# Performance work log

Measured on AMD Instinct MI355X. Metric: run time of the kernel, lower is better.

Reference implementation:

```python
import jax, jax.numpy as jnp
import numpy as np

N, E = 50000, 1600000
IN_DIM, HID, L, H = 300, 256, 3, 4
HD = HID // H  # 64
EPS = 1e-5


def setup_inputs() -> dict:
    key = jax.random.key(0)
    ks = jax.random.split(key, 24)
    s = 0.02
    inp = {
        'node_feats': jax.random.normal(ks[0], (N, IN_DIM), jnp.float32),
        'role': jax.random.randint(ks[1], (N,), 0, 3),
        'edge_src': jax.random.randint(ks[2], (E,), 0, N),
        'edge_dst': jax.random.randint(ks[3], (E,), 0, N),
        'edge_weights': jax.random.uniform(ks[4], (E,), jnp.float32),
        # input role transforms (question / entity / context)
        'Wq': jax.random.normal(ks[5], (IN_DIM, HID), jnp.float32) * s,
        'bq': jnp.zeros((HID,), jnp.float32),
        'We': jax.random.normal(ks[6], (IN_DIM, HID), jnp.float32) * s,
        'be': jnp.zeros((HID,), jnp.float32),
        'Wc': jax.random.normal(ks[7], (IN_DIM, HID), jnp.float32) * s,
        'bc': jnp.zeros((HID,), jnp.float32),
        # per-head value projections [H, HID, HD] (q/k projections omitted:
        # softmax over a scalar == 1.0, so they never affect output or grads)
        'Wv': jax.random.normal(ks[8], (H, HID, HD), jnp.float32) * s,
        'bv': jnp.zeros((H, HD), jnp.float32),
        # shared 'default' edge-type transform (the torch code always falls
        # through to 'default' because edata['rel'] entries are tensors)
        'Wd': jax.random.normal(ks[9], (HD, HD), jnp.float32) * s,
        'bd': jnp.zeros((HD,), jnp.float32),
        # attention_output
        'Wo': jax.random.normal(ks[10], (HID, HID), jnp.float32) * s,
        'bo': jnp.zeros((HID,), jnp.float32),
        # GRUCell params (torch layout: [3*HID, in], gate order r,z,n)
        'W_ih': jax.random.normal(ks[11], (3 * HID, HID), jnp.float32) * s,
        'W_hh': jax.random.normal(ks[12], (3 * HID, HID), jnp.float32) * s,
        'b_ih': jnp.zeros((3 * HID,), jnp.float32),
        'b_hh': jnp.zeros((3 * HID,), jnp.float32),
        # per-layer LayerNorm affine params [L, HID]
        'ln_w': jnp.ones((L, HID), jnp.float32),
        'ln_b': jnp.zeros((L, HID), jnp.float32),
    }
    return inp


def _layernorm(x, w, b):
    mu = jnp.mean(x, -1, keepdims=True)
    var = jnp.mean(jnp.square(x - mu), -1, keepdims=True)
    return (x - mu) * jax.lax.rsqrt(var + EPS) * w + b


def _gru_cell(x, hprev, W_ih, W_hh, b_ih, b_hh):
    gi = x @ W_ih.T + b_ih
    gh = hprev @ W_hh.T + b_hh
    i_r, i_z, i_n = jnp.split(gi, 3, axis=-1)
    h_r, h_z, h_n = jnp.split(gh, 3, axis=-1)
    r = jax.nn.sigmoid(i_r + h_r)
    z = jax.nn.sigmoid(i_z + h_z)
    n = jnp.tanh(i_n + r * h_n)
    return (1.0 - z) * n + z * hprev


def reference(node_feats, role, edge_src, edge_dst, edge_weights,
              Wq, bq, We, be, Wc, bc, Wv, bv, Wd, bd, Wo, bo,
              W_ih, W_hh, b_ih, b_hh, ln_w, ln_b):
    n_nodes = node_feats.shape[0]
    # role-dependent input transform: 0=question, 1=evidence/answer, 2=other
    hq = node_feats @ Wq + bq
    he = node_feats @ We + be
    hc = node_feats @ Wc + bc
    r = role[:, None]
    h = jax.nn.relu(jnp.where(r == 0, hq, jnp.where(r == 1, he, hc)))

    path_mem = jax.lax.stop_gradient(h)  # .detach().clone()
    prev_h = h
    num_layers, num_heads = ln_w.shape[0], Wv.shape[0]
    for layer in range(num_layers):
        head_msgs = []
        for hd in range(num_heads):
            # value proj + shared 'default' edge transform (node-level, fused)
            vt = (h @ Wv[hd] + bv[hd]) @ Wd + bd  # [N, HD]
            # scalar softmax == 1.0 -> attn_weight == edge_weight
            msg = vt[edge_src] * edge_weights[:, None]  # [E, HD]
            head_msgs.append(jax.ops.segment_sum(msg, edge_dst,
                                                 num_segments=n_nodes))
        combined = jnp.concatenate(head_msgs, axis=-1)  # [N, HID]
        path_mem = _gru_cell(combined, path_mem, W_ih, W_hh, b_ih, b_hh)
        h = _layernorm(prev_h + combined @ Wo + bo, ln_w[layer], ln_b[layer])
        # dropout: identity in eval mode
        prev_h = h
    return h + path_mem
```

## Files before the change

### kernel.cpp

```cpp
#include <hip/hip_runtime.h>
#include <math.h>

#define NN 50000
#define EE 1600000
#define IND 300
#define KPAD 320
#define NL 3
#define NBLK 785
#define AGG_NB 12500

typedef unsigned short u16;
typedef __attribute__((ext_vector_type(8))) short short8;
typedef __attribute__((ext_vector_type(4))) float floatx4;

__device__ __forceinline__ float b2f(u16 u) {
  union { unsigned i; float f; } v; v.i = ((unsigned)u) << 16; return v.f;
}
__device__ __forceinline__ u16 f2b(float f) {
  union { unsigned i; float f; } v; v.f = f;
  unsigned b = v.i; b += 0x7fffu + ((b >> 16) & 1u);
  return (u16)(b >> 16);
}
__device__ __forceinline__ float sigf(float x) { return 1.0f / (1.0f + __expf(-x)); }

__global__ void count_kernel(const int* __restrict__ dst, int* __restrict__ cnt) {
  int e = blockIdx.x * 256 + threadIdx.x;
  if (e < EE) atomicAdd(&cnt[dst[e]], 1);
}

__global__ __launch_bounds__(256) void scan1_kernel(const int* __restrict__ cnt,
                                                    int* __restrict__ rs,
                                                    int* __restrict__ bsum) {
  __shared__ int ws[4];
  const int t = threadIdx.x, l = t & 63, w = t >> 6;
  const int base = blockIdx.x * 2048 + t * 8;
  int v[8];
  int tot = 0;
  #pragma unroll
  for (int k = 0; k < 8; ++k) {
    int i = base + k;
    v[k] = (i < NN) ? cnt[i] : 0;
    tot += v[k];
  }
  int x = tot;
  #pragma unroll
  for (int off = 1; off < 64; off <<= 1) {
    int y = __shfl_up(x, off);
    if (l >= off) x += y;
  }
  if (l == 63) ws[w] = x;
  __syncthreads();
  int wpre = 0;
  for (int q = 0; q < w; ++q) wpre += ws[q];
  int run = wpre + (x - tot);
  #pragma unroll
  for (int k = 0; k < 8; ++k) {
    int i = base + k;
    if (i < NN) rs[i] = run;
    run += v[k];
  }
  if (t == 255) bsum[blockIdx.x] = wpre + x;
}

__global__ void scan2_kernel(int* __restrict__ bsum, int nb) {
  int l = threadIdx.x;
  int v = (l < nb) ? bsum[l] : 0;
  int x = v;
  #pragma unroll
  for (int off = 1; off < 64; off <<= 1) {
    int y = __shfl_up(x, off);
    if (l >= off) x += y;
  }
  if (l < nb) bsum[l] = x - v;
  if (l == 63) bsum[nb] = x;
}

__global__ void scan3_kernel(const int* __restrict__ bsum, int* __restrict__ rs, int nb) {
  int i = blockIdx.x * 256 + threadIdx.x;
  if (i < NN) rs[i] += bsum[i >> 11];
  if (i == 0) rs[NN] = bsum[nb];
}

__global__ void fill_kernel(const int* __restrict__ dst, const int* __restrict__ rs,
                            int* __restrict__ ncnt, const int* __restrict__ esrc,
                            const float* __restrict__ ew, int2* __restrict__ srcw) {
  int e = blockIdx.x * 256 + threadIdx.x;
  if (e < EE) {
    int d = dst[e];
    int p = atomicAdd(&ncnt[d], 1);
    int2 v;
    v.x = esrc[e];
    v.y = __float_as_int(ew[e]);
    srcw[rs[d] + p] = v;
  }
}

__global__ void role_count(const int* __restrict__ role, int* __restrict__ cnt3) {
  __shared__ int lc[3];
  if (threadIdx.x < 3) lc[threadIdx.x] = 0;
  __syncthreads();
  int i = blockIdx.x * 256 + threadIdx.x;
  if (i < NN) atomicAdd(&lc[role[i]], 1);
  __syncthreads();
  if (threadIdx.x < 3) atomicAdd(&cnt3[threadIdx.x], lc[threadIdx.x]);
}

__global__ void role_plan(const int* __restrict__ cnt3, int* __restrict__ pbase,
                          int* __restrict__ blkrole) {
  __shared__ int pb[4];
  if (threadIdx.x == 0) {
    pb[0] = 0;
    for (int b = 0; b < 3; ++b) pb[b + 1] = pb[b] + (((cnt3[b] + 63) >> 6) << 6);
    for (int b = 0; b < 4; ++b) pbase[b] = pb[b];
  }
  __syncthreads();
  for (int blk = threadIdx.x; blk < NBLK; blk += 256) {
    int m0 = blk * 64;
    int r = -1;
    for (int b = 0; b < 3; ++b)
      if (m0 >= pb[b] && m0 < pb[b + 1]) r = b;
    blkrole[blk] = r;
  }
}

__global__ void role_fill(const int* __restrict__ role, const int* __restrict__ pbase,
                          int* __restrict__ pos3, int* __restrict__ perm) {
  __shared__ int lcnt[3], lbase[3];
  int i = blockIdx.x * 256 + threadIdx.x;
  if (threadIdx.x < 3) lcnt[threadIdx.x] = 0;
  __syncthreads();
  int r = 0, lr = 0;
  bool valid = (i < NN);
  if (valid) {
    r = role[i];
    lr = atomicAdd(&lcnt[r], 1);
  }
  __syncthreads();
  if (threadIdx.x < 3) lbase[threadIdx.x] = atomicAdd(&pos3[threadIdx.x], lcnt[threadIdx.x]);
  __syncthreads();
  if (valid) perm[pbase[r] + lbase[r] + lr] = i;
}

__global__ void xcast_kernel(const float* __restrict__ X, u16* __restrict__ Xb) {
  size_t i = (size_t)blockIdx.x * 256 + threadIdx.x;
  if (i >= (size_t)NN * KPAD) return;
  int r = (int)(i / KPAD), k = (int)(i % KPAD);
  Xb[i] = (k < IND) ? f2b(X[(size_t)r * IND + k]) : (u16)0;
}

__global__ void wt3_kernel(const float* __restrict__ Wq, const float* __restrict__ We,
                           const float* __restrict__ Wc, u16* __restrict__ Wqt,
                           u16* __restrict__ Wet, u16* __restrict__ Wct) {
  int n = blockIdx.x;
  int which = blockIdx.y;
  const float* W = (which == 0) ? Wq : (which == 1) ? We : Wc;
  u16* Wt = (which == 0) ? Wqt : (which == 1) ? Wet : Wct;
  for (int k = threadIdx.x; k < KPAD; k += 256)
    Wt[(size_t)n * KPAD + k] = (k < IND) ? f2b(W[(size_t)k * 256 + n]) : (u16)0;
}

__global__ void wallt_kernel(const float* __restrict__ Wv, const float* __restrict__ Wd,
                             u16* __restrict__ Wallt) {
  int i = blockIdx.x;
  int c = threadIdx.x;
  int hd = c >> 6, j = c & 63;
  const float* wv = &Wv[hd * (256 * 64) + i * 64];
  float s = 0.f;
  #pragma unroll
  for (int m = 0; m < 64; ++m) s = fmaf(wv[m], Wd[m * 64 + j], s);
  Wallt[(size_t)c * 256 + i] = f2b(s);
}

__global__ void ball_kernel(const float* __restrict__ bv, const float* __restrict__ Wd,
                            const float* __restrict__ bd, float* __restrict__ ball) {
  int c = threadIdx.x;
  int hd = c >> 6, j = c & 63;
  float s = bd[j];
  #pragma unroll
  for (int m = 0; m < 64; ++m) s = fmaf(bv[hd * 64 + m], Wd[m * 64 + j], s);
  ball[c] = s;
}

__global__ void wot_kernel(const float* __restrict__ Wo, u16* __restrict__ Wot) {
  int n = blockIdx.x;
  int k = threadIdx.x;
  Wot[(size_t)n * 256 + k] = f2b(Wo[(size_t)k * 256 + n]);
}

__global__ void castbf2_kernel(const float* __restrict__ s0, const float* __restrict__ s1,
                               u16* __restrict__ d0, u16* __restrict__ d1) {
  int i = blockIdx.x * 256 + threadIdx.x;
  const int n = 768 * 256;
  if (i < n) d0[i] = f2b(s0[i]);
  else if (i < 2 * n) d1[i - n] = f2b(s1[i - n]);
}

#define GEMM_PROLOG \
  __shared__ __align__(16) u16 As[64][72]; \
  __shared__ __align__(16) u16 Bs[64][72]; \
  const int t = threadIdx.x; \
  const int lane = t & 63; \
  const int wv_ = t >> 6; \
  const int wr = wv_ >> 1, wc = wv_ & 1; \
  const int l15 = lane & 15, l4 = lane >> 4; \
  const int srow = t >> 2; \
  const int scol = (t & 3) << 4;

#define STAGE_A(AG, ASTRIDE, VALID, ROWIDX, K0) { \
  int4 v0 = {0, 0, 0, 0}, v1 = {0, 0, 0, 0}; \
  if (VALID) { \
    const int4* p_ = (const int4*)&(AG)[(size_t)(ROWIDX) * (ASTRIDE) + (K0) + scol]; \
    v0 = p_[0]; v1 = p_[1]; \
  } \
  *(int4*)&As[srow][scol] = v0; \
  *(int4*)&As[srow][scol + 8] = v1; }

#define STAGE_B(BG, BSTRIDE, ROWIDX, K0) { \
  const int4* p_ = (const int4*)&(BG)[(size_t)(ROWIDX) * (BSTRIDE) + (K0) + scol]; \
  *(int4*)&Bs[srow][scol] = p_[0]; \
  *(int4*)&Bs[srow][scol + 8] = p_[1]; }

#define MFMA_STEP(ACC) { \
  _Pragma("unroll") \
  for (int kc = 0; kc < 2; ++kc) { \
    short8 a0_ = *(const short8*)&As[wr * 32 + 0 + l15][kc * 32 + l4 * 8]; \
    short8 a1_ = *(const short8*)&As[wr * 32 + 16 + l15][kc * 32 + l4 * 8]; \
    short8 b0_ = *(const short8*)&Bs[wc * 32 + 0 + l15][kc * 32 + l4 * 8]; \
    short8 b1_ = *(const short8*)&Bs[wc * 32 + 16 + l15][kc * 32 + l4 * 8]; \
    ACC[0][0] = __builtin_amdgcn_mfma_f32_16x16x32_bf16(a0_, b0_, ACC[0][0], 0, 0, 0); \
    ACC[0][1] = __builtin_amdgcn_mfma_f32_16x16x32_bf16(a0_, b1_, ACC[0][1], 0, 0, 0); \
    ACC[1][0] = __builtin_amdgcn_mfma_f32_16x16x32_bf16(a1_, b0_, ACC[1][0], 0, 0, 0); \
    ACC[1][1] = __builtin_amdgcn_mfma_f32_16x16x32_bf16(a1_, b1_, ACC[1][1], 0, 0, 0); \
  } }

#define GEMM128_PROLOG \
  __shared__ __align__(16) u16 As[128][72]; \
  __shared__ __align__(16) u16 Bs[128][72]; \
  const int t = threadIdx.x; \
  const int lane = t & 63; \
  const int wv_ = t >> 6; \
  const int qr = (wv_ >> 1) * 64, qc = (wv_ & 1) * 64; \
  const int l15 = lane & 15, l4 = lane >> 4; \
  const int srow = t >> 1; \
  const int scol = (t & 1) * 32;

#define STAGE128_A(AG, ASTRIDE, VALID, ROWIDX, K0) { \
  int4 v0 = {0,0,0,0}, v1 = {0,0,0,0}, v2 = {0,0,0,0}, v3 = {0,0,0,0}; \
  if (VALID) { \
    const int4* p_ = (const int4*)&(AG)[(size_t)(ROWIDX) * (ASTRIDE) + (K0) + scol]; \
    v0 = p_[0]; v1 = p_[1]; v2 = p_[2]; v3 = p_[3]; \
  } \
  *(int4*)&As[srow][scol] = v0; *(int4*)&As[srow][scol + 8] = v1; \
  *(int4*)&As[srow][scol + 16] = v2; *(int4*)&As[srow][scol + 24] = v3; }

#define STAGE128_B(BG, BSTRIDE, ROWIDX, K0) { \
  const int4* p_ = (const int4*)&(BG)[(size_t)(ROWIDX) * (BSTRIDE) + (K0) + scol]; \
  *(int4*)&Bs[srow][scol] = p_[0]; *(int4*)&Bs[srow][scol + 8] = p_[1]; \
  *(int4*)&Bs[srow][scol + 16] = p_[2]; *(int4*)&Bs[srow][scol + 24] = p_[3]; }

#define MFMA128_STEP(ACC) { \
  _Pragma("unroll") \
  for (int kc = 0; kc < 2; ++kc) { \
    short8 af_[4], bf_[4]; \
    _Pragma("unroll") \
    for (int m = 0; m < 4; ++m) af_[m] = *(const short8*)&As[qr + m * 16 + l15][kc * 32 + l4 * 8]; \
    _Pragma("unroll") \
    for (int n = 0; n < 4; ++n) bf_[n] = *(const short8*)&Bs[qc + n * 16 + l15][kc * 32 + l4 * 8]; \
    _Pragma("unroll") \
    for (int m = 0; m < 4; ++m) \
      _Pragma("unroll") \
      for (int n = 0; n < 4; ++n) \
        ACC[m][n] = __builtin_amdgcn_mfma_f32_16x16x32_bf16(af_[m], bf_[n], ACC[m][n], 0, 0, 0); \
  } }

__global__ __launch_bounds__(256) void proj_mfma(
    const u16* __restrict__ Xb, const int* __restrict__ perm,
    const int* __restrict__ blkrole,
    const u16* __restrict__ Wqt, const u16* __restrict__ Wet, const u16* __restrict__ Wct,
    const float* __restrict__ bq, const float* __restrict__ be, const float* __restrict__ bc,
    u16* __restrict__ h, u16* __restrict__ pm) {
  const int brole = blkrole[blockIdx.y];
  if (brole < 0) return;
  GEMM_PROLOG
  const int m0 = blockIdx.y * 64;
  const int n0 = blockIdx.x * 64;
  const u16* Bt = (brole == 0) ? Wqt : (brole == 1) ? Wet : Wct;
  const float* bb = (brole == 0) ? bq : (brole == 1) ? be : bc;
  const int prow = perm[m0 + srow];
  floatx4 acc[2][2] = {};
  for (int k0 = 0; k0 < KPAD; k0 += 64) {
    STAGE_A(Xb, KPAD, prow >= 0, prow, k0)
    STAGE_B(Bt, KPAD, n0 + srow, k0)
    __syncthreads();
    MFMA_STEP(acc)
    __syncthreads();
  }
  #pragma unroll
  for (int m = 0; m < 2; ++m)
    #pragma unroll
    for (int reg = 0; reg < 4; ++reg) {
      int gr = m0 + wr * 32 + m * 16 + l4 * 4 + reg;
      int pr = perm[gr];
      if (pr >= 0) {
        #pragma unroll
        for (int n = 0; n < 2; ++n) {
          int c = n0 + wc * 32 + n * 16 + l15;
          float vo = fmaxf(acc[m][n][reg] + bb[c], 0.f);
          u16 ub = f2b(vo);
          h[(size_t)pr * 256 + c] = ub;
          pm[(size_t)pr * 256 + c] = ub;
        }
      }
    }
}

__global__ __launch_bounds__(256) void vgemm_mfma(
    const u16* __restrict__ A, const u16* __restrict__ Bt,
    const float* __restrict__ bias, u16* __restrict__ Vs) {
  GEMM128_PROLOG
  const int m0 = blockIdx.y * 128;
  const int n0 = blockIdx.x * 128;
  const int ar = m0 + srow;
  floatx4 acc[4][4] = {};
  for (int k0 = 0; k0 < 256; k0 += 64) {
    STAGE128_A(A, 256, ar < NN, ar, k0)
    STAGE128_B(Bt, 256, n0 + srow, k0)
    __syncthreads();
    MFMA128_STEP(acc)
    __syncthreads();
  }
  #pragma unroll
  for (int m = 0; m < 4; ++m)
    #pragma unroll
    for (int reg = 0; reg < 4; ++reg) {
      int gr = m0 + qr + m * 16 + l4 * 4 + reg;
      if (gr < NN) {
        #pragma unroll
        for (int n = 0; n < 4; ++n) {
          int c = n0 + qc + n * 16 + l15;
          size_t off = ((size_t)(c >> 5) * NN + gr) * 32 + (c & 31);
          Vs[off] = f2b(acc[m][n][reg] + bias[c]);
        }
      }
    }
}

__global__ __launch_bounds__(256) void agg_kernel(
    const int2* __restrict__ srcw, const int* __restrict__ rs,
    const u16* __restrict__ Vs, u16* __restrict__ comb) {
  int bid = blockIdx.x;
  int slice = bid / AGG_NB;
  int nb = bid - slice * AGG_NB;
  int n = nb * 4 + (threadIdx.x >> 6);
  int lane = threadIdx.x & 63;
  int hh = lane >> 5;
  int u = lane & 31;
  int s = rs[n], e = rs[n + 1];
  const u16* __restrict__ vbase = Vs + (size_t)slice * NN * 32;
  float a0 = 0.f, a1 = 0.f, a2 = 0.f, a3 = 0.f;
  for (int base = s; base < e; base += 64) {
    int2 p = {0, 0};
    if (base + lane < e) p = srcw[base + lane];
    int cnt = min(64, e - base);
    for (int k = 0; k < cnt; k += 8) {
      int j0 = k + hh, j1 = k + 2 + hh, j2 = k + 4 + hh, j3 = k + 6 + hh;
      int s0 = __shfl(p.x, j0 & 63), s1 = __shfl(p.x, j1 & 63);
      int s2 = __shfl(p.x, j2 & 63), s3 = __shfl(p.x, j3 & 63);
      int w0i = __shfl(p.y, j0 & 63), w1i = __shfl(p.y, j1 & 63);
      int w2i = __shfl(p.y, j2 & 63), w3i = __shfl(p.y, j3 & 63);
      bool v0 = j0 < cnt, v1 = j1 < cnt, v2 = j2 < cnt, v3 = j3 < cnt;
      float w0 = v0 ? __int_as_float(w0i) : 0.f;
      float w1 = v1 ? __int_as_float(w1i) : 0.f;
      float w2 = v2 ? __int_as_float(w2i) : 0.f;
      float w3 = v3 ? __int_as_float(w3i) : 0.f;
      s0 = v0 ? s0 : 0; s1 = v1 ? s1 : 0;
      s2 = v2 ? s2 : 0; s3 = v3 ? s3 : 0;
      float f0 = b2f(vbase[(size_t)s0 * 32 + u]);
      float f1 = b2f(vbase[(size_t)s1 * 32 + u]);
      float f2 = b2f(vbase[(size_t)s2 * 32 + u]);
      float f3 = b2f(vbase[(size_t)s3 * 32 + u]);
      a0 = fmaf(w0, f0, a0); a1 = fmaf(w1, f1, a1);
      a2 = fmaf(w2, f2, a2); a3 = fmaf(w3, f3, a3);
    }
  }
  float a = (a0 + a1) + (a2 + a3);
  a += __shfl_xor(a, 32);
  if (hh == 0) comb[(size_t)n * 256 + slice * 32 + u] = f2b(a);
}

__global__ __launch_bounds__(256) void gru_mfma(
    const u16* __restrict__ comb, const u16* __restrict__ pmc,
    const u16* __restrict__ Wiht, const u16* __restrict__ Whht,
    const float* __restrict__ bih, const float* __restrict__ bhh,
    u16* __restrict__ pmn) {
  __shared__ __align__(16) u16 As[2][64][72];
  __shared__ __align__(16) u16 Bs[6][64][72];
  const int t = threadIdx.x;
  const int lane = t & 63;
  const int wv_ = t >> 6;
  const int wr = wv_ >> 1, wc = wv_ & 1;
  const int l15 = lane & 15, l4 = lane >> 4;
  const int srow = t >> 2;
  const int scol = (t & 3) << 4;
  const int m0 = blockIdx.y * 64;
  const int cb = blockIdx.x;
  const int ar = m0 + srow;
  const bool av = ar < NN;
  floatx4 acc[6][2][2] = {};
  for (int k0 = 0; k0 < 256; k0 += 64) {
    {
      int4 v0 = {0,0,0,0}, v1 = {0,0,0,0}, u0 = {0,0,0,0}, u1 = {0,0,0,0};
      if (av) {
        const int4* pa = (const int4*)&comb[(size_t)ar * 256 + k0 + scol];
        v0 = pa[0]; v1 = pa[1];
        const int4* pb = (const int4*)&pmc[(size_t)ar * 256 + k0 + scol];
        u0 = pb[0]; u1 = pb[1];
      }
      *(int4*)&As[0][srow][scol] = v0; *(int4*)&As[0][srow][scol + 8] = v1;
      *(int4*)&As[1][srow][scol] = u0; *(int4*)&As[1][srow][scol + 8] = u1;
    }
    #pragma unroll
    for (int g = 0; g < 3; ++g) {
      size_t row = (size_t)(g * 256 + cb * 64 + srow);
      const int4* p1 = (const int4*)&Wiht[row * 256 + k0 + scol];
      *(int4*)&Bs[g][srow][scol] = p1[0];
      *(int4*)&Bs[g][srow][scol + 8] = p1[1];
      const int4* p2 = (const int4*)&Whht[row * 256 + k0 + scol];
      *(int4*)&Bs[3 + g][srow][scol] = p2[0];
      *(int4*)&Bs[3 + g][srow][scol + 8] = p2[1];
    }
    __syncthreads();
    #pragma unroll
    for (int kc = 0; kc < 2; ++kc) {
      short8 a0f[2], a1f[2];
      #pragma unroll
      for (int m = 0; m < 2; ++m) {
        a0f[m] = *(const short8*)&As[0][wr * 32 + m * 16 + l15][kc * 32 + l4 * 8];
        a1f[m] = *(const short8*)&As[1][wr * 32 + m * 16 + l15][kc * 32 + l4 * 8];
      }
      #pragma unroll
      for (int g = 0; g < 3; ++g) {
        short8 b0 = *(const short8*)&Bs[g][wc * 32 + 0 + l15][kc * 32 + l4 * 8];
        short8 b1 = *(const short8*)&Bs[g][wc * 32 + 16 + l15][kc * 32 + l4 * 8];
        acc[g][0][0] = __builtin_amdgcn_mfma_f32_16x16x32_bf16(a0f[0], b0, acc[g][0][0], 0, 0, 0);
        acc[g][0][1] = __builtin_amdgcn_mfma_f32_16x16x32_bf16(a0f[0], b1, acc[g][0][1], 0, 0, 0);
        acc[g][1][0] = __builtin_amdgcn_mfma_f32_16x16x32_bf16(a0f[1], b0, acc[g][1][0], 0, 0, 0);
        acc[g][1][1] = __builtin_amdgcn_mfma_f32_16x16x32_bf16(a0f[1], b1, acc[g][1][1], 0, 0, 0);
      }
      #pragma unroll
      for (int g = 3; g < 6; ++g) {
        short8 b0 = *(const short8*)&Bs[g][wc * 32 + 0 + l15][kc * 32 + l4 * 8];
        short8 b1 = *(const short8*)&Bs[g][wc * 32 + 16 + l15][kc * 32 + l4 * 8];
        acc[g][0][0] = __builtin_amdgcn_mfma_f32_16x16x32_bf16(a1f[0], b0, acc[g][0][0], 0, 0, 0);
        acc[g][0][1] = __builtin_amdgcn_mfma_f32_16x16x32_bf16(a1f[0], b1, acc[g][0][1], 0, 0, 0);
        acc[g][1][0] = __builtin_amdgcn_mfma_f32_16x16x32_bf16(a1f[1], b0, acc[g][1][0], 0, 0, 0);
        acc[g][1][1] = __builtin_amdgcn_mfma_f32_16x16x32_bf16(a1f[1], b1, acc[g][1][1], 0, 0, 0);
      }
    }
    __syncthreads();
  }
  #pragma unroll
  for (int m = 0; m < 2; ++m)
    #pragma unroll
    for (int reg = 0; reg < 4; ++reg) {
      int gr = m0 + wr * 32 + m * 16 + l4 * 4 + reg;
      if (gr < NN) {
        #pragma unroll
        for (int n = 0; n < 2; ++n) {
          int c = cb * 64 + wc * 32 + n * 16 + l15;
          float r = sigf(acc[0][m][n][reg] + acc[3][m][n][reg] + bih[c] + bhh[c]);
          float z = sigf(acc[1][m][n][reg] + acc[4][m][n][reg] + bih[256 + c] + bhh[256 + c]);
          float i_n = acc[2][m][n][reg] + bih[512 + c];
          float h_n = acc[5][m][n][reg] + bhh[512 + c];
          float nn2 = tanhf(i_n + r * h_n);
          float po = b2f(pmc[(size_t)gr * 256 + c]);
          pmn[(size_t)gr * 256 + c] = f2b((1.f - z) * nn2 + z * po);
        }
      }
    }
}

__global__ __launch_bounds__(256) void wo_mfma(
    const u16* __restrict__ comb, const u16* __restrict__ Wot,
    const float* __restrict__ bo, const u16* __restrict__ h,
    u16* __restrict__ tmp) {
  GEMM128_PROLOG
  const int m0 = blockIdx.y * 128;
  const int n0 = blockIdx.x * 128;
  const int ar = m0 + srow;
  floatx4 acc[4][4] = {};
  for (int k0 = 0; k0 < 256; k0 += 64) {
    STAGE128_A(comb, 256, ar < NN, ar, k0)
    STAGE128_B(Wot, 256, n0 + srow, k0)
    __syncthreads();
    MFMA128_STEP(acc)
    __syncthreads();
  }
  #pragma unroll
  for (int m = 0; m < 4; ++m)
    #pragma unroll
    for (int reg = 0; reg < 4; ++reg) {
      int gr = m0 + qr + m * 16 + l4 * 4 + reg;
      if (gr < NN) {
        #pragma unroll
        for (int n = 0; n < 4; ++n) {
          int c = n0 + qc + n * 16 + l15;
          float v = acc[m][n][reg] + bo[c] + b2f(h[(size_t)gr * 256 + c]);
          tmp[(size_t)gr * 256 + c] = f2b(v);
        }
      }
    }
}

__global__ __launch_bounds__(256) void ln_kernel(
    const u16* __restrict__ tmp, u16* __restrict__ h,
    const float* __restrict__ lnw, const float* __restrict__ lnb) {
  int n = blockIdx.x * 4 + (threadIdx.x >> 6);
  int l = threadIdx.x & 63;
  if (n >= NN) return;
  ushort4 v = *(const ushort4*)&tmp[(size_t)n * 256 + l * 4];
  float x0 = b2f(v.x), x1 = b2f(v.y), x2 = b2f(v.z), x3 = b2f(v.w);
  float s = x0 + x1 + x2 + x3;
  #pragma unroll
  for (int off = 1; off < 64; off <<= 1) s += __shfl_xor(s, off);
  float mu = s * (1.f / 256.f);
  float d0 = x0 - mu, d1 = x1 - mu, d2 = x2 - mu, d3 = x3 - mu;
  float vs = d0 * d0 + d1 * d1 + d2 * d2 + d3 * d3;
  #pragma unroll
  for (int off = 1; off < 64; off <<= 1) vs += __shfl_xor(vs, off);
  float inv = rsqrtf(vs * (1.f / 256.f) + 1e-5f);
  int c = l * 4;
  ushort4 o;
  o.x = f2b(d0 * inv * lnw[c + 0] + lnb[c + 0]);
  o.y = f2b(d1 * inv * lnw[c + 1] + lnb[c + 1]);
  o.z = f2b(d2 * inv * lnw[c + 2] + lnb[c + 2]);
  o.w = f2b(d3 * inv * lnw[c + 3] + lnb[c + 3]);
  *(ushort4*)&h[(size_t)n * 256 + c] = o;
}

__global__ __launch_bounds__(256) void ln_final_kernel(
    const u16* __restrict__ tmp, const u16* __restrict__ pm,
    const float* __restrict__ lnw, const float* __restrict__ lnb,
    float* __restrict__ out) {
  int n = blockIdx.x * 4 + (threadIdx.x >> 6);
  int l = threadIdx.x & 63;
  if (n >= NN) return;
  ushort4 v = *(const ushort4*)&tmp[(size_t)n * 256 + l * 4];
  float x0 = b2f(v.x), x1 = b2f(v.y), x2 = b2f(v.z), x3 = b2f(v.w);
  float s = x0 + x1 + x2 + x3;
  #pragma unroll
  for (int off = 1; off < 64; off <<= 1) s += __shfl_xor(s, off);
  float mu = s * (1.f / 256.f);
  float d0 = x0 - mu, d1 = x1 - mu, d2 = x2 - mu, d3 = x3 - mu;
  float vs = d0 * d0 + d1 * d1 + d2 * d2 + d3 * d3;
  #pragma unroll
  for (int off = 1; off < 64; off <<= 1) vs += __shfl_xor(vs, off);
  float inv = rsqrtf(vs * (1.f / 256.f) + 1e-5f);
  int c = l * 4;
  ushort4 pv = *(const ushort4*)&pm[(size_t)n * 256 + c];
  float4 o;
  o.x = b2f(f2b(d0 * inv * lnw[c + 0] + lnb[c + 0])) + b2f(pv.x);
  o.y = b2f(f2b(d1 * inv * lnw[c + 1] + lnb[c + 1])) + b2f(pv.y);
  o.z = b2f(f2b(d2 * inv * lnw[c + 2] + lnb[c + 2])) + b2f(pv.z);
  o.w = b2f(f2b(d3 * inv * lnw[c + 3] + lnb[c + 3])) + b2f(pv.w);
  *(float4*)&out[(size_t)n * 256 + c] = o;
}

extern "C" void kernel_launch(void* const* d_in, const int* in_sizes, int n_in,
                              void* d_out, int out_size, void* d_ws, size_t ws_size,
                              hipStream_t stream) {
  const float* node_feats = (const float*)d_in[0];
  const int* role = (const int*)d_in[1];
  const int* esrc = (const int*)d_in[2];
  const int* edst = (const int*)d_in[3];
  const float* ew = (const float*)d_in[4];
  const float* Wq = (const float*)d_in[5];
  const float* bq = (const float*)d_in[6];
  const float* We = (const float*)d_in[7];
  const float* be = (const float*)d_in[8];
  const float* Wc = (const float*)d_in[9];
  const float* bc = (const float*)d_in[10];
  const float* Wv = (const float*)d_in[11];
  const float* bv = (const float*)d_in[12];
  const float* Wd = (const float*)d_in[13];
  const float* bd = (const float*)d_in[14];
  const float* Wo = (const float*)d_in[15];
  const float* bo = (const float*)d_in[16];
  const float* Wih = (const float*)d_in[17];
  const float* Whh = (const float*)d_in[18];
  const float* bih = (const float*)d_in[19];
  const float* bhh = (const float*)d_in[20];
  const float* lnw = (const float*)d_in[21];
  const float* lnb = (const float*)d_in[22];
  float* out = (float*)d_out;

  char* ws = (char*)d_ws;
  size_t off = 0;
  auto take = [&](size_t bytes) {
    char* p = ws + off;
    off = (off + bytes + 511) & ~(size_t)511;
    return p;
  };
  const size_t NC2 = (size_t)NN * 256 * 2;
  u16* Xb = (u16*)take((size_t)NN * KPAD * 2);
  u16* h = (u16*)take(NC2);
  u16* pm0 = (u16*)take(NC2);
  u16* pm1 = (u16*)take(NC2);
  u16* Vs = (u16*)take(NC2);
  u16* comb = (u16*)take(NC2);
  u16* tmp = (u16*)take(NC2);
  u16* Wqt = (u16*)take((size_t)256 * KPAD * 2);
  u16* Wet = (u16*)take((size_t)256 * KPAD * 2);
  u16* Wct = (u16*)take((size_t)256 * KPAD * 2);
  u16* Wallt = (u16*)take((size_t)256 * 256 * 2);
  u16* Wot = (u16*)take((size_t)256 * 256 * 2);
  u16* Wiht = (u16*)take((size_t)768 * 256 * 2);
  u16* Whht = (u16*)take((size_t)768 * 256 * 2);
  float* ball = (float*)take(256 * 4);
  int* cnt = (int*)take((size_t)NN * 4);
  int* rs = (int*)take((size_t)(NN + 1) * 4);
  int* ncnt = (int*)take((size_t)NN * 4);
  int2* srcw = (int2*)take((size_t)EE * 8);
  int* cnt3 = (int*)take(16);
  int* pos3 = (int*)take(16);
  int* pbase = (int*)take(16);
  int* blkrole = (int*)take((size_t)NBLK * 4);
  int* perm = (int*)take((size_t)NBLK * 64 * 4);
  int* bsum = (int*)take(64 * 4);

  const int NB_SCAN = (NN + 2047) / 2048;

  hipMemsetAsync(cnt, 0, (size_t)NN * 4, stream);
  hipMemsetAsync(ncnt, 0, (size_t)NN * 4, stream);
  hipMemsetAsync(cnt3, 0, 16, stream);
  hipMemsetAsync(pos3, 0, 16, stream);
  hipMemsetAsync(perm, 0xFF, (size_t)NBLK * 64 * 4, stream);

  count_kernel<<<(EE + 255) / 256, 256, 0, stream>>>(edst, cnt);
  scan1_kernel<<<NB_SCAN, 256, 0, stream>>>(cnt, rs, bsum);
  scan2_kernel<<<1, 64, 0, stream>>>(bsum, NB_SCAN);
  scan3_kernel<<<(NN + 255) / 256, 256, 0, stream>>>(bsum, rs, NB_SCAN);
  fill_kernel<<<(EE + 255) / 256, 256, 0, stream>>>(edst, rs, ncnt, esrc, ew, srcw);

  role_count<<<(NN + 255) / 256, 256, 0, stream>>>(role, cnt3);
  role_plan<<<1, 256, 0, stream>>>(cnt3, pbase, blkrole);
  role_fill<<<(NN + 255) / 256, 256, 0, stream>>>(role, pbase, pos3, perm);

  xcast_kernel<<<(int)(((size_t)NN * KPAD + 255) / 256), 256, 0, stream>>>(node_feats, Xb);
  wt3_kernel<<<dim3(256, 3), 256, 0, stream>>>(Wq, We, Wc, Wqt, Wet, Wct);
  wallt_kernel<<<256, 256, 0, stream>>>(Wv, Wd, Wallt);
  ball_kernel<<<1, 256, 0, stream>>>(bv, Wd, bd, ball);
  wot_kernel<<<256, 256, 0, stream>>>(Wo, Wot);
  castbf2_kernel<<<(2 * 768 * 256 + 255) / 256, 256, 0, stream>>>(Wih, Whh, Wiht, Whht);

  proj_mfma<<<dim3(4, NBLK), 256, 0, stream>>>(Xb, perm, blkrole, Wqt, Wet, Wct,
                                               bq, be, bc, h, pm0);

  u16* pmc = pm0;
  u16* pmn = pm1;
  const int MB128 = (NN + 127) / 128;
  const int MB64 = (NN + 63) / 64;
  for (int layer = 0; layer < NL; ++layer) {
    vgemm_mfma<<<dim3(2, MB128), 256, 0, stream>>>(h, Wallt, ball, Vs);
    agg_kernel<<<8 * AGG_NB, 256, 0, stream>>>(srcw, rs, Vs, comb);
    gru_mfma<<<dim3(4, MB64), 256, 0, stream>>>(comb, pmc, Wiht, Whht, bih, bhh, pmn);
    wo_mfma<<<dim3(2, MB128), 256, 0, stream>>>(comb, Wot, bo, h, tmp);
    if (layer < NL - 1) {
      ln_kernel<<<(NN + 3) / 4, 256, 0, stream>>>(tmp, h, lnw + layer * 256, lnb + layer * 256);
    } else {
      ln_final_kernel<<<(NN + 3) / 4, 256, 0, stream>>>(tmp, pmn, lnw + layer * 256,
                                                        lnb + layer * 256, out);
    }
    u16* sw = pmc; pmc = pmn; pmn = sw;
  }
}
```

Before: 1.289 ms.

## Pack edge src and bf16 weight into 32 bits and vectorize aggregation gathers

New measurement: 1.110 ms. 13.9% less time.

```diff
diff --git a/kernel.cpp b/kernel.cpp
--- a/kernel.cpp
+++ b/kernel.cpp
@@ -10,6 +10,7 @@
 #define AGG_NB 12500
 
 typedef unsigned short u16;
+typedef unsigned int u32;
 typedef __attribute__((ext_vector_type(8))) short short8;
 typedef __attribute__((ext_vector_type(4))) float floatx4;
 
@@ -83,14 +84,12 @@
 
 __global__ void fill_kernel(const int* __restrict__ dst, const int* __restrict__ rs,
                             int* __restrict__ ncnt, const int* __restrict__ esrc,
-                            const float* __restrict__ ew, int2* __restrict__ srcw) {
+                            const float* __restrict__ ew, u32* __restrict__ srcw) {
   int e = blockIdx.x * 256 + threadIdx.x;
   if (e < EE) {
     int d = dst[e];
     int p = atomicAdd(&ncnt[d], 1);
-    int2 v;
-    v.x = esrc[e];
-    v.y = __float_as_int(ew[e]);
+    u32 v = ((u32)f2b(ew[e]) << 16) | (u32)esrc[e];
     srcw[rs[d] + p] = v;
   }
 }
@@ -346,46 +345,56 @@
 }
 
 __global__ __launch_bounds__(256) void agg_kernel(
-    const int2* __restrict__ srcw, const int* __restrict__ rs,
+    const u32* __restrict__ srcw, const int* __restrict__ rs,
     const u16* __restrict__ Vs, u16* __restrict__ comb) {
+  __shared__ u32 meta[4][64];
   int bid = blockIdx.x;
   int slice = bid / AGG_NB;
   int nb = bid - slice * AGG_NB;
-  int n = nb * 4 + (threadIdx.x >> 6);
+  int wid = threadIdx.x >> 6;
+  int n = nb * 4 + wid;
   int lane = threadIdx.x & 63;
-  int hh = lane >> 5;
-  int u = lane & 31;
+  int q = lane >> 4;
+  int u = lane & 15;
   int s = rs[n], e = rs[n + 1];
   const u16* __restrict__ vbase = Vs + (size_t)slice * NN * 32;
-  float a0 = 0.f, a1 = 0.f, a2 = 0.f, a3 = 0.f;
+  float a0 = 0.f, a1 = 0.f, b0 = 0.f, b1 = 0.f;
   for (int base = s; base < e; base += 64) {
-    int2 p = {0, 0};
-    if (base + lane < e) p = srcw[base + lane];
+    u32 m = 0;
+    if (base + lane < e) m = srcw[base + lane];
+    meta[wid][lane] = m;
     int cnt = min(64, e - base);
-    for (int k = 0; k < cnt; k += 8) {
-      int j0 = k + hh, j1 = k + 2 + hh, j2 = k + 4 + hh, j3 = k + 6 + hh;
-      int s0 = __shfl(p.x, j0 & 63), s1 = __shfl(p.x, j1 & 63);
-      int s2 = __shfl(p.x, j2 & 63), s3 = __shfl(p.x, j3 & 63);
-      int w0i = __shfl(p.y, j0 & 63), w1i = __shfl(p.y, j1 & 63);
-      int w2i = __shfl(p.y, j2 & 63), w3i = __shfl(p.y, j3 & 63);
-      bool v0 = j0 < cnt, v1 = j1 < cnt, v2 = j2 < cnt, v3 = j3 < cnt;
-      float w0 = v0 ? __int_as_float(w0i) : 0.f;
-      float w1 = v1 ? __int_as_float(w1i) : 0.f;
-      float w2 = v2 ? __int_as_float(w2i) : 0.f;
-      float w3 = v3 ? __int_as_float(w3i) : 0.f;
-      s0 = v0 ? s0 : 0; s1 = v1 ? s1 : 0;
-      s2 = v2 ? s2 : 0; s3 = v3 ? s3 : 0;
-      float f0 = b2f(vbase[(size_t)s0 * 32 + u]);
-      float f1 = b2f(vbase[(size_t)s1 * 32 + u]);
-      float f2 = b2f(vbase[(size_t)s2 * 32 + u]);
-      float f3 = b2f(vbase[(size_t)s3 * 32 + u]);
-      a0 = fmaf(w0, f0, a0); a1 = fmaf(w1, f1, a1);
-      a2 = fmaf(w2, f2, a2); a3 = fmaf(w3, f3, a3);
-    }
-  }
-  float a = (a0 + a1) + (a2 + a3);
-  a += __shfl_xor(a, 32);
-  if (hh == 0) comb[(size_t)n * 256 + slice * 32 + u] = f2b(a);
+    for (int k = 0; k < cnt; k += 16) {
+      u32 m0 = meta[wid][k + q];
+      u32 m1 = meta[wid][k + 4 + q];
+      u32 m2 = meta[wid][k + 8 + q];
+      u32 m3 = meta[wid][k + 12 + q];
+      float w0 = __int_as_float((int)(m0 & 0xffff0000u));
+      float w1 = __int_as_float((int)(m1 & 0xffff0000u));
+      float w2 = __int_as_float((int)(m2 & 0xffff0000u));
+      float w3 = __int_as_float((int)(m3 & 0xffff0000u));
+      u32 p0 = *(const u32*)&vbase[(size_t)(m0 & 0xffffu) * 32 + u * 2];
+      u32 p1 = *(const u32*)&vbase[(size_t)(m1 & 0xffffu) * 32 + u * 2];
+      u32 p2 = *(const u32*)&vbase[(size_t)(m2 & 0xffffu) * 32 + u * 2];
+      u32 p3 = *(const u32*)&vbase[(size_t)(m3 & 0xffffu) * 32 + u * 2];
+      a0 = fmaf(w0, __int_as_float((int)(p0 << 16)), a0);
+      a1 = fmaf(w0, __int_as_float((int)(p0 & 0xffff0000u)), a1);
+      b0 = fmaf(w1, __int_as_float((int)(p1 << 16)), b0);
+      b1 = fmaf(w1, __int_as_float((int)(p1 & 0xffff0000u)), b1);
+      a0 = fmaf(w2, __int_as_float((int)(p2 << 16)), a0);
+      a1 = fmaf(w2, __int_as_float((int)(p2 & 0xffff0000u)), a1);
+      b0 = fmaf(w3, __int_as_float((int)(p3 << 16)), b0);
+      b1 = fmaf(w3, __int_as_float((int)(p3 & 0xffff0000u)), b1);
+    }
+  }
+  a0 += b0; a1 += b1;
+  a0 += __shfl_xor(a0, 16); a0 += __shfl_xor(a0, 32);
+  a1 += __shfl_xor(a1, 16); a1 += __shfl_xor(a1, 32);
+  if (q == 0) {
+    ushort2 o;
+    o.x = f2b(a0); o.y = f2b(a1);
+    *(ushort2*)&comb[(size_t)n * 256 + slice * 32 + u * 2] = o;
+  }
 }
 
 __global__ __launch_bounds__(256) void gru_mfma(
@@ -620,7 +629,7 @@
   int* cnt = (int*)take((size_t)NN * 4);
   int* rs = (int*)take((size_t)(NN + 1) * 4);
   int* ncnt = (int*)take((size_t)NN * 4);
-  int2* srcw = (int2*)take((size_t)EE * 8);
+  u32* srcw = (u32*)take((size_t)EE * 4);
   int* cnt3 = (int*)take(16);
   int* pos3 = (int*)take(16);
   int* pbase = (int*)take(16);
```
